# Performance work log

Hardware: AMD Instinct MI355X
Metric: run time of the kernel (lower is better)

## Reference

```python
import jax, jax.numpy as jnp
import numpy as np

N = 50000
E = 600000
IN_DIM = 128
D = 32          # out_dim per head
H = 4           # heads
M = 3           # num metapaths
HID = 128       # semantic attention hidden
NEG_SLOPE = 0.2


def setup_inputs() -> dict:
    key = jax.random.key(0)
    ks = jax.random.split(key, 12)
    x = jax.random.normal(ks[0], (N, IN_DIM), dtype=jnp.float32)
    mp_edge_index = jax.random.randint(ks[1], (M, 2, E), 0, N, dtype=jnp.int64)
    s = 1.0 / np.sqrt(IN_DIM)
    W = jax.random.normal(ks[2], (M, IN_DIM, H * D), dtype=jnp.float32) * s
    att_src = jax.random.normal(ks[3], (M, H, D), dtype=jnp.float32) * (1.0 / np.sqrt(D))
    att_dst = jax.random.normal(ks[4], (M, H, D), dtype=jnp.float32) * (1.0 / np.sqrt(D))
    bias = jnp.zeros((M, H * D), dtype=jnp.float32)
    ln_gamma = jnp.ones((H * D,), dtype=jnp.float32)
    ln_beta = jnp.zeros((H * D,), dtype=jnp.float32)
    sem_W1 = jax.random.normal(ks[5], (H * D, HID), dtype=jnp.float32) * (1.0 / np.sqrt(H * D))
    sem_b1 = jnp.zeros((HID,), dtype=jnp.float32)
    sem_W2 = jax.random.normal(ks[6], (HID, 1), dtype=jnp.float32) * (1.0 / np.sqrt(HID))
    return dict(x=x, mp_edge_index=mp_edge_index, W=W, att_src=att_src,
                att_dst=att_dst, bias=bias, ln_gamma=ln_gamma, ln_beta=ln_beta,
                sem_W1=sem_W1, sem_b1=sem_b1, sem_W2=sem_W2)


def _gat_conv(x, edge_index, W_m, a_src, a_dst, b_m):
    # PyG GATConv (add_self_loops=True, concat=True). x: [N, F_in]
    n = x.shape[0]
    h = (x @ W_m).reshape(n, H, D)                       # [N, H, D]
    loops = jnp.arange(n, dtype=edge_index.dtype)
    src = jnp.concatenate([edge_index[0], loops])        # [E+N]
    dst = jnp.concatenate([edge_index[1], loops])
    alpha_s = jnp.einsum('nhd,hd->nh', h, a_src)         # [N, H]
    alpha_d = jnp.einsum('nhd,hd->nh', h, a_dst)
    e = jax.nn.leaky_relu(alpha_s[src] + alpha_d[dst], NEG_SLOPE)  # [E+N, H]
    # segment softmax over edges grouped by destination node
    e_max = jax.ops.segment_max(e, dst, num_segments=n)
    e = jnp.exp(e - e_max[dst])
    denom = jax.ops.segment_sum(e, dst, num_segments=n)
    alpha = e / (denom[dst] + 1e-16)                     # [E+N, H]
    msg = h[src] * alpha[:, :, None]                     # [E+N, H, D]
    out = jax.ops.segment_sum(msg, dst, num_segments=n)  # [N, H, D]
    return out.reshape(n, H * D) + b_m


def _layer_norm(y, gamma, beta):
    mu = y.mean(-1, keepdims=True)
    var = y.var(-1, keepdims=True)
    return (y - mu) * jax.lax.rsqrt(var + 1e-5) * gamma + beta


def reference(x, mp_edge_index, W, att_src, att_dst, bias, ln_gamma, ln_beta,
              sem_W1, sem_b1, sem_W2):
    embs = []
    for i in range(M):
        emb = _gat_conv(x, mp_edge_index[i], W[i], att_src[i], att_dst[i], bias[i])
        emb = jax.nn.elu(_layer_norm(emb, ln_gamma, ln_beta))
        embs.append(emb)
    z = jnp.stack(embs, axis=1)                          # [N, M, H*D]
    # semantic attention
    w = (jnp.tanh(z @ sem_W1 + sem_b1) @ sem_W2).mean(0)  # [M, 1]
    beta = jax.nn.softmax(w, axis=0)                      # [M, 1]
    out_emb = (beta[None, :, :] * z).sum(1)               # [N, H*D]
    att_mp = beta.squeeze()                               # [M]
    return out_emb, att_mp
```

## Files before the change

kernel.cpp:

```cpp
#include <hip/hip_runtime.h>
#include <hip/hip_bf16.h>

#define N_NODES 50000
#define N_EDGES 600000
#define NMETA   3
#define LTOT (NMETA * N_NODES)
#define SPAN_SHIFT 9
#define NBUCK 98
#define BCAP 8192
#define NCHUNK 147
#define NABLK 782
#define NSLOT (NMETA * NBUCK * BCAP)
#define LOG2E 1.4426950408889634f

typedef unsigned short u16;
typedef short bf16x8 __attribute__((ext_vector_type(8)));
typedef float f32x4 __attribute__((ext_vector_type(4)));

__device__ __forceinline__ float bf2f(u16 v) {
    union { unsigned int u; float f; } x; x.u = ((unsigned int)v) << 16; return x.f;
}
__device__ __forceinline__ float u2f(unsigned int u) {
    union { unsigned int u; float f; } x; x.u = u; return x.f;
}
__device__ __forceinline__ u16 f2bf(float f) {
    return __hip_bfloat16_raw(__float2bfloat16(f)).x;
}

__global__ __launch_bounds__(256) void k_build1(
    const int* __restrict__ ei, int* __restrict__ gcnt,
    unsigned long long* __restrict__ pairs,
    const float* __restrict__ W, const float* __restrict__ W1,
    u16* __restrict__ WT, u16* __restrict__ W1T)
{
    const int bid = blockIdx.x;
    const int t = threadIdx.x;
    if (bid >= NMETA * NCHUNK) {
        int idx = (bid - NMETA * NCHUNK) * 256 + t;
        if (idx < NMETA * 16384) {
            int m = idx >> 14, r = idx & 16383;
            int col = r >> 7, k = r & 127;
            WT[idx] = f2bf(W[(m << 14) + k * 128 + col]);
        } else {
            int r = idx - NMETA * 16384;
            int col = r >> 7, k = r & 127;
            W1T[r] = f2bf(W1[k * 128 + col]);
        }
        return;
    }
    const int m = bid / NCHUNK;
    const int e0 = (bid % NCHUNK) * 4096;
    __shared__ int cnt[NBUCK];
    __shared__ int gbase[NBUCK];
    if (t < NBUCK) cnt[t] = 0;
    __syncthreads();
    const int* srcp = ei + (size_t)m * 2 * N_EDGES;
    const int* dstp = srcp + N_EDGES;
    int sa[16], da[16], sl[16];
    #pragma unroll
    for (int j = 0; j < 16; ++j) {
        int e = e0 + j * 256 + t;
        if (e < N_EDGES) {
            int s = srcp[e], d = dstp[e];
            if ((unsigned)s >= N_NODES) s = 0;
            if ((unsigned)d >= N_NODES) d = 0;
            sa[j] = s; da[j] = d;
            sl[j] = atomicAdd(&cnt[d >> SPAN_SHIFT], 1);
        } else sl[j] = -1;
    }
    __syncthreads();
    if (t < NBUCK) gbase[t] = atomicAdd(&gcnt[m * NBUCK + t], cnt[t]);
    __syncthreads();
    #pragma unroll
    for (int j = 0; j < 16; ++j) {
        if (sl[j] < 0) continue;
        int b = da[j] >> SPAN_SHIFT;
        int pos = gbase[b] + sl[j];
        if (pos < BCAP)
            pairs[(size_t)(m * NBUCK + b) * BCAP + pos] =
                ((unsigned long long)(da[j] & 511) << 32) | (unsigned)(sa[j] * 128);
    }
}

__global__ __launch_bounds__(256) void k_build2(
    const int* __restrict__ gcnt, const unsigned long long* __restrict__ pairs,
    int* __restrict__ row_start, int* __restrict__ row_end, int* __restrict__ eidx,
    int* __restrict__ ptot,
    const float* __restrict__ x, const u16* __restrict__ WT,
    const float* __restrict__ att_src, const float* __restrict__ att_dst,
    u16* __restrict__ h, float* __restrict__ alpha_s, float* __restrict__ alpha_d)
{
    const int bid = blockIdx.x;
    const int t = threadIdx.x;
    if (bid < NMETA * NBUCK) {
        const int m = bid / NBUCK, b = bid % NBUCK;
        __shared__ int cnt[512];
        __shared__ int off[512];
        __shared__ int wsum[4];
        int nb = gcnt[m * NBUCK + b]; if (nb > BCAP) nb = BCAP;
        const int base = (m * NBUCK + b) * BCAP;
        cnt[t] = 0; cnt[t + 256] = 0;
        __syncthreads();
        for (int e = t; e < nb; e += 256) {
            int dl = (int)(pairs[(size_t)base + e] >> 32);
            atomicAdd(&cnt[dl], 1);
        }
        __syncthreads();
        int c0 = cnt[2 * t], c1 = cnt[2 * t + 1];
        int v0p = (c0 + 3) & ~3, v1p = (c1 + 3) & ~3;
        int s = v0p + v1p;
        int lane = t & 63, wv = t >> 6;
        int incl = s;
        #pragma unroll
        for (int o = 1; o < 64; o <<= 1) {
            int u = __shfl_up(incl, o);
            if (lane >= o) incl += u;
        }
        if (lane == 63) wsum[wv] = incl;
        __syncthreads();
        int woff = 0;
        for (int i = 0; i < wv; ++i) woff += wsum[i];
        int ex = woff + incl - s;
        off[2 * t] = ex;
        off[2 * t + 1] = ex + v0p;
        if (t == 255) {
            int tot = ex + v0p + v1p;
            ptot[m * NBUCK + b] = tot < BCAP ? tot : BCAP;
        }
        for (int q = ex + c0; q < ex + v0p && q < BCAP; ++q) eidx[base + q] = 0;
        for (int q = ex + v0p + c1; q < ex + v0p + v1p && q < BCAP; ++q) eidx[base + q] = 0;
        __syncthreads();
        const int node0 = b << SPAN_SHIFT;
        for (int i = t; i < 512; i += 256) {
            int n = node0 + i;
            if (n < N_NODES) {
                int st = base + off[i];
                row_start[m * N_NODES + n] = st;
                row_end[m * N_NODES + n]   = st + cnt[i];
            }
        }
        __syncthreads();
        for (int e = t; e < nb; e += 256) {
            unsigned long long p = pairs[(size_t)base + e];
            int dl = (int)(p >> 32);
            int pos = atomicAdd(&off[dl], 1);
            if (pos >= BCAP) continue;
            eidx[base + pos] = (dl << 23) | (int)(unsigned)p;
        }
        return;
    }
    const int g = bid - NMETA * NBUCK;
    const int bx = g % NABLK, m = g / NABLK;
    const int wv = t >> 6, lane = t & 63;
    const int row0 = (bx * 4 + wv) * 16;
    if (row0 >= N_NODES) return;
    const int lhi = lane >> 4, llo = lane & 15;
    const float* xrow = x + (size_t)(row0 + llo) * 128 + lhi * 8;
    bf16x8 a[4];
    #pragma unroll
    for (int ks = 0; ks < 4; ++ks) {
        float4 f0 = *(const float4*)(xrow + ks * 32);
        float4 f1 = *(const float4*)(xrow + ks * 32 + 4);
        bf16x8 av;
        av[0] = f2bf(f0.x); av[1] = f2bf(f0.y); av[2] = f2bf(f0.z); av[3] = f2bf(f0.w);
        av[4] = f2bf(f1.x); av[5] = f2bf(f1.y); av[6] = f2bf(f1.z); av[7] = f2bf(f1.w);
        a[ks] = av;
    }
    const u16* wbase = WT + (size_t)m * 16384 + (size_t)llo * 128 + lhi * 8;
    u16* hm = h + ((size_t)m * N_NODES + row0) * 128;
    float sp[4][4], dp[4][4];
    #pragma unroll
    for (int i = 0; i < 4; ++i)
        #pragma unroll
        for (int r = 0; r < 4; ++r) { sp[i][r] = 0.f; dp[i][r] = 0.f; }
    #pragma unroll
    for (int cf = 0; cf < 8; ++cf) {
        f32x4 acc = {0.f, 0.f, 0.f, 0.f};
        const u16* wp = wbase + cf * 16 * 128;
        #pragma unroll
        for (int ks = 0; ks < 4; ++ks) {
            bf16x8 bb = *(const bf16x8*)(wp + ks * 32);
            acc = __builtin_amdgcn_mfma_f32_16x16x32_bf16(a[ks], bb, acc, 0, 0, 0);
        }
        const int col = cf * 16 + llo;
        const int hh = cf >> 1;
        const float as = att_src[m * 128 + col];
        const float adv = att_dst[m * 128 + col];
        #pragma unroll
        for (int r = 0; r < 4; ++r) {
            hm[(size_t)(lhi * 4 + r) * 128 + col] = f2bf(acc[r]);
            sp[hh][r] += acc[r] * as;
            dp[hh][r] += acc[r] * adv;
        }
    }
    #pragma unroll
    for (int o = 1; o <= 8; o <<= 1) {
        #pragma unroll
        for (int i = 0; i < 4; ++i)
            #pragma unroll
            for (int r = 0; r < 4; ++r) {
                sp[i][r] += __shfl_xor(sp[i][r], o);
                dp[i][r] += __shfl_xor(dp[i][r], o);
            }
    }
    if (llo == 0) {
        #pragma unroll
        for (int r = 0; r < 4; ++r) {
            int n = row0 + lhi * 4 + r;
            f32x4 vs = {sp[0][r] * LOG2E, sp[1][r] * LOG2E, sp[2][r] * LOG2E, sp[3][r] * LOG2E};
            f32x4 vd = {dp[0][r] * LOG2E, dp[1][r] * LOG2E, dp[2][r] * LOG2E, dp[3][r] * LOG2E};
            *(f32x4*)(alpha_s + ((size_t)m * N_NODES + n) * 4) = vs;
            *(f32x4*)(alpha_d + ((size_t)m * N_NODES + n) * 4) = vd;
        }
    }
}

__global__ __launch_bounds__(256) void k_ew(
    const int* __restrict__ ptot, int* __restrict__ eidx,
    const float* __restrict__ alpha_s, const float* __restrict__ alpha_d,
    u16* __restrict__ ew)
{
    for (int sidx = blockIdx.x * 256 + threadIdx.x; sidx < NSLOT; sidx += gridDim.x * 256) {
        const int bucket = sidx >> 13;
        const int i = sidx & (BCAP - 1);
        if (i >= ptot[bucket]) continue;
        const int m = bucket / NBUCK, b = bucket % NBUCK;
        const int node0 = b << SPAN_SHIFT;
        int v = eidx[sidx];
        int src128 = v & 0x7FFFFF;
        int dl = (unsigned)v >> 23;
        const float* as_m = alpha_s + (size_t)m * N_NODES * 4;
        const float* ad_m = alpha_d + (size_t)m * N_NODES * 4;
        f32x4 as4 = *(const f32x4*)(as_m + (src128 >> 5));
        f32x4 ad4 = *(const f32x4*)(ad_m + (size_t)(node0 + dl) * 4);
        u16* ewp = ew + (size_t)(sidx >> 2) * 16 + (sidx & 3);
        #pragma unroll
        for (int k = 0; k < 4; ++k) {
            float pre = as4[k] + ad4[k];
            pre = fmaxf(pre, 0.2f * pre);
            ewp[k * 4] = f2bf(exp2f(pre));
        }
        eidx[sidx] = src128 * 2;
    }
}

__global__ __launch_bounds__(256) void k_gather(
    const int* __restrict__ row_start, const int* __restrict__ row_end,
    const int* __restrict__ eidx, const u16* __restrict__ ew,
    const float* __restrict__ alpha_s, const float* __restrict__ alpha_d,
    const u16* __restrict__ h,
    const float* __restrict__ bias, const float* __restrict__ gamma,
    const float* __restrict__ lbeta,
    u16* __restrict__ z)
{
    long long w = ((long long)blockIdx.x * blockDim.x + threadIdx.x) >> 6;
    if (w >= (long long)LTOT) return;
    int m = (int)(w / N_NODES), n = (int)(w % N_NODES);
    int lane = threadIdx.x & 63, hh = lane >> 4;
    const char* h_m = (const char*)(h + (size_t)m * N_NODES * 128);
    const char* ewb = (const char*)ew;
    const int lb = lane * 4;
    const float* as_m = alpha_s + (size_t)m * N_NODES * 4;
    const float* ad_m = alpha_d + (size_t)m * N_NODES * 4;
    float pre = as_m[n * 4 + hh] + ad_m[n * 4 + hh];
    pre = fmaxf(pre, 0.2f * pre);
    float ev = exp2f(pre);
    float esum = ev;
    ushort2 hv = *(const ushort2*)(h_m + (size_t)n * 256 + lb);
    float acc0 = ev * bf2f(hv.x), acc1 = ev * bf2f(hv.y);
    int p = row_start[m * N_NODES + n];
    const int end = row_end[m * N_NODES + n];
    for (; p + 3 < end; p += 4) {
        int4 o4 = *(const int4*)(eidx + p);
        uint2 ewv = *(const uint2*)(ewb + (size_t)(p + hh) * 8);
        float e1 = u2f(ewv.x << 16), e2 = u2f(ewv.x & 0xffff0000u);
        float e3 = u2f(ewv.y << 16), e4 = u2f(ewv.y & 0xffff0000u);
        ushort2 h1 = *(const ushort2*)(h_m + o4.x + lb);
        ushort2 h2 = *(const ushort2*)(h_m + o4.y + lb);
        ushort2 h3 = *(const ushort2*)(h_m + o4.z + lb);
        ushort2 h4 = *(const ushort2*)(h_m + o4.w + lb);
        esum += (e1 + e2) + (e3 + e4);
        acc0 += e1 * bf2f(h1.x) + e2 * bf2f(h2.x) + e3 * bf2f(h3.x) + e4 * bf2f(h4.x);
        acc1 += e1 * bf2f(h1.y) + e2 * bf2f(h2.y) + e3 * bf2f(h3.y) + e4 * bf2f(h4.y);
    }
    for (; p < end; ++p) {
        int o1 = eidx[p];
        float e1 = bf2f(*(const u16*)(ewb + (size_t)((p & ~3) + hh) * 8 + (p & 3) * 2));
        ushort2 h1 = *(const ushort2*)(h_m + o1 + lb);
        esum += e1;
        acc0 += e1 * bf2f(h1.x);
        acc1 += e1 * bf2f(h1.y);
    }
    float rinv = 1.f / (esum + 1e-16f);
    float v0 = acc0 * rinv + bias[m * 128 + lane * 2];
    float v1 = acc1 * rinv + bias[m * 128 + lane * 2 + 1];
    float s1 = v0 + v1, s2 = v0 * v0 + v1 * v1;
    #pragma unroll
    for (int o = 32; o >= 1; o >>= 1) { s1 += __shfl_xor(s1, o); s2 += __shfl_xor(s2, o); }
    float mu = s1 * (1.f / 128.f);
    float var = s2 * (1.f / 128.f) - mu * mu;
    float rs = rsqrtf(var + 1e-5f);
    float o0 = (v0 - mu) * rs * gamma[lane * 2]     + lbeta[lane * 2];
    float o1 = (v1 - mu) * rs * gamma[lane * 2 + 1] + lbeta[lane * 2 + 1];
    o0 = o0 > 0.f ? o0 : (__expf(o0) - 1.f);
    o1 = o1 > 0.f ? o1 : (__expf(o1) - 1.f);
    ushort2 outv; outv.x = f2bf(o0); outv.y = f2bf(o1);
    *(ushort2*)(z + ((size_t)n * NMETA + m) * 128 + lane * 2) = outv;
}

__global__ __launch_bounds__(256) void k_sem(
    const u16* __restrict__ z, const u16* __restrict__ W1T,
    const float* __restrict__ b1, const float* __restrict__ W2,
    float* __restrict__ wpart)
{
    __shared__ float part[NMETA];
    const int t = threadIdx.x;
    if (t < NMETA) part[t] = 0.f;
    __syncthreads();
    const int wv = t >> 6, lane = t & 63;
    const int row0 = (blockIdx.x * 4 + wv) * 16;
    if (row0 < LTOT) {
        const int lhi = lane >> 4, llo = lane & 15;
        const u16* zrow = z + (size_t)(row0 + llo) * 128 + lhi * 8;
        bf16x8 a[4];
        #pragma unroll
        for (int ks = 0; ks < 4; ++ks) a[ks] = *(const bf16x8*)(zrow + ks * 32);
        const u16* wb = W1T + (size_t)llo * 128 + lhi * 8;
        float rowacc[4] = {0.f, 0.f, 0.f, 0.f};
        #pragma unroll
        for (int cf = 0; cf < 8; ++cf) {
            f32x4 acc = {0.f, 0.f, 0.f, 0.f};
            const u16* wp = wb + cf * 16 * 128;
            #pragma unroll
            for (int ks = 0; ks < 4; ++ks) {
                bf16x8 bb = *(const bf16x8*)(wp + ks * 32);
                acc = __builtin_amdgcn_mfma_f32_16x16x32_bf16(a[ks], bb, acc, 0, 0, 0);
            }
            int col = cf * 16 + llo;
            float b1v = b1[col], w2v = W2[col];
            #pragma unroll
            for (int r = 0; r < 4; ++r)
                rowacc[r] += tanhf(acc[r] + b1v) * w2v;
        }
        #pragma unroll
        for (int o = 1; o <= 8; o <<= 1) {
            #pragma unroll
            for (int r = 0; r < 4; ++r) rowacc[r] += __shfl_xor(rowacc[r], o);
        }
        if (llo == 0) {
            #pragma unroll
            for (int r = 0; r < 4; ++r)
                atomicAdd(&part[(row0 + lhi * 4 + r) % NMETA], rowacc[r]);
        }
    }
    __syncthreads();
    if (t < NMETA) atomicAdd(&wpart[t], part[t]);
}

__global__ void k_beta(const float* __restrict__ wpart, float* __restrict__ betab,
                       float* __restrict__ attout)
{
    if (threadIdx.x == 0 && blockIdx.x == 0) {
        float w0 = wpart[0] * (1.f / N_NODES);
        float w1 = wpart[1] * (1.f / N_NODES);
        float w2 = wpart[2] * (1.f / N_NODES);
        float mx = fmaxf(w0, fmaxf(w1, w2));
        float e0 = __expf(w0 - mx), e1 = __expf(w1 - mx), e2 = __expf(w2 - mx);
        float s = 1.f / (e0 + e1 + e2);
        float b0 = e0 * s, b1 = e1 * s, b2 = e2 * s;
        betab[0] = b0; betab[1] = b1; betab[2] = b2;
        attout[0] = b0; attout[1] = b1; attout[2] = b2;
    }
}

__global__ __launch_bounds__(256) void k_combine(
    const u16* __restrict__ z, const float* __restrict__ betab,
    float* __restrict__ out)
{
    int idx = blockIdx.x * blockDim.x + threadIdx.x;
    if (idx >= N_NODES * 64) return;
    int n = idx >> 6, c2 = (idx & 63) * 2;
    float b0 = betab[0], b1 = betab[1], b2 = betab[2];
    const u16* zp = z + (size_t)n * NMETA * 128 + c2;
    ushort2 a0 = *(const ushort2*)(zp);
    ushort2 a1 = *(const ushort2*)(zp + 128);
    ushort2 a2 = *(const ushort2*)(zp + 256);
    float2 ov;
    ov.x = b0 * bf2f(a0.x) + b1 * bf2f(a1.x) + b2 * bf2f(a2.x);
    ov.y = b0 * bf2f(a0.y) + b1 * bf2f(a1.y) + b2 * bf2f(a2.y);
    *(float2*)(out + (size_t)n * 128 + c2) = ov;
}

extern "C" void kernel_launch(void* const* d_in, const int* in_sizes, int n_in,
                              void* d_out, int out_size, void* d_ws, size_t ws_size,
                              hipStream_t stream) {
    const float* x       = (const float*)d_in[0];
    const int*   ei      = (const int*)d_in[1];
    const float* W       = (const float*)d_in[2];
    const float* att_src = (const float*)d_in[3];
    const float* att_dst = (const float*)d_in[4];
    const float* bias    = (const float*)d_in[5];
    const float* gamma   = (const float*)d_in[6];
    const float* lbeta   = (const float*)d_in[7];
    const float* W1      = (const float*)d_in[8];
    const float* b1      = (const float*)d_in[9];
    const float* W2      = (const float*)d_in[10];

    char* ws = (char*)d_ws;
    size_t off = 0;
    int* gcnt    = (int*)(ws + off);  off += sizeof(int) * 512;
    int* ptot    = (int*)(ws + off);  off += sizeof(int) * 512;
    float* wpart = (float*)(ws + off);
    float* betab = wpart + 8;         off += 64;
    const size_t zero_bytes = off;
    off = (off + 255) & ~(size_t)255;
    int* row_start = (int*)(ws + off); off += sizeof(int) * 150016;
    int* row_end   = (int*)(ws + off); off += sizeof(int) * 150016;
    u16* h      = (u16*)(ws + off);    off += sizeof(u16) * (size_t)NMETA * N_NODES * 128;
    float* alpha_s = (float*)(ws + off); off += sizeof(float) * (size_t)LTOT * 4;
    float* alpha_d = (float*)(ws + off); off += sizeof(float) * (size_t)LTOT * 4;
    u16* WT     = (u16*)(ws + off);    off += sizeof(u16) * (size_t)NMETA * 128 * 128;
    u16* W1T    = (u16*)(ws + off);    off += sizeof(u16) * (size_t)128 * 128;
    int* eidx   = (int*)(ws + off);    off += sizeof(int) * (size_t)NSLOT;
    u16* ew     = (u16*)(ws + off);    off += sizeof(u16) * (size_t)NSLOT * 4;
    unsigned long long* pairs = (unsigned long long*)(ws + off);
    u16* z = (u16*)(ws + off);
    off += sizeof(u16) * (size_t)N_NODES * NMETA * 128;
    if (ws_size < off) return;

    hipMemsetAsync(d_ws, 0, zero_bytes, stream);

    k_build1<<<dim3(NMETA * NCHUNK + 256), 256, 0, stream>>>(ei, gcnt, pairs, W, W1, WT, W1T);
    k_build2<<<dim3(NMETA * NBUCK + NABLK * NMETA), 256, 0, stream>>>(
        gcnt, pairs, row_start, row_end, eidx, ptot,
        x, WT, att_src, att_dst, h, alpha_s, alpha_d);
    k_ew<<<dim3(2048), 256, 0, stream>>>(ptot, eidx, alpha_s, alpha_d, ew);
    k_gather<<<dim3((LTOT + 3) / 4), 256, 0, stream>>>(row_start, row_end, eidx, ew,
                                                       alpha_s, alpha_d, h,
                                                       bias, gamma, lbeta, z);
    k_sem<<<dim3((LTOT / 16 + 3) / 4), 256, 0, stream>>>(z, W1T, b1, W2, wpart);
    k_beta<<<1, 64, 0, stream>>>(wpart, betab, (float*)d_out + (size_t)N_NODES * 128);
    k_combine<<<dim3((N_NODES * 64 + 255) / 256), 256, 0, stream>>>(z, betab, (float*)d_out);
}
```

Baseline: 279.8 us.

## Pack edge pairs to 32-bit, use bf16 dot2 in gather, fuse beta into semantic kernel

Edge pairs shrink from 64-bit to 32-bit words with the destination-local index pre-shifted, so the bucket sort reads half the bytes and no longer rebuilds the index. The gather loop uses packed bf16 dot2 instructions with byte permutes in place of scalar converts and multiplies. The semantic kernel swaps tanhf for an exp2-based tanh and computes the softmax beta in the last block through an atomic completion counter, removing a separate launch. The combine kernel switches to 16-byte vector loads and stores. The dot2 path accumulates in a different order and the fast tanh is slightly less accurate.

```diff
diff --git a/kernel.cpp b/kernel.cpp
--- a/kernel.cpp
+++ b/kernel.cpp
@@ -11,6 +11,7 @@
 #define NCHUNK 147
 #define NABLK 782
 #define NSLOT (NMETA * NBUCK * BCAP)
+#define NSEMBLK ((LTOT / 16 + 3) / 4)
 #define LOG2E 1.4426950408889634f
 
 typedef unsigned short u16;
@@ -27,9 +28,20 @@
     return __hip_bfloat16_raw(__float2bfloat16(f)).x;
 }
 
+#if __has_builtin(__builtin_amdgcn_fdot2_f32_bf16)
+#define HAS_DOT2 1
+typedef __bf16 bf16x2v __attribute__((ext_vector_type(2)));
+__device__ __forceinline__ float dot2bf(unsigned hp, unsigned ep, float acc) {
+    return __builtin_amdgcn_fdot2_f32_bf16(
+        __builtin_bit_cast(bf16x2v, hp), __builtin_bit_cast(bf16x2v, ep), acc, false);
+}
+#else
+#define HAS_DOT2 0
+#endif
+
 __global__ __launch_bounds__(256) void k_build1(
     const int* __restrict__ ei, int* __restrict__ gcnt,
-    unsigned long long* __restrict__ pairs,
+    unsigned* __restrict__ pairs,
     const float* __restrict__ W, const float* __restrict__ W1,
     u16* __restrict__ WT, u16* __restrict__ W1T)
 {
@@ -78,12 +90,12 @@
         int pos = gbase[b] + sl[j];
         if (pos < BCAP)
             pairs[(size_t)(m * NBUCK + b) * BCAP + pos] =
-                ((unsigned long long)(da[j] & 511) << 32) | (unsigned)(sa[j] * 128);
+                ((unsigned)(da[j] & 511) << 23) | (unsigned)(sa[j] * 128);
     }
 }
 
 __global__ __launch_bounds__(256) void k_build2(
-    const int* __restrict__ gcnt, const unsigned long long* __restrict__ pairs,
+    const int* __restrict__ gcnt, const unsigned* __restrict__ pairs,
     int* __restrict__ row_start, int* __restrict__ row_end, int* __restrict__ eidx,
     int* __restrict__ ptot,
     const float* __restrict__ x, const u16* __restrict__ WT,
@@ -102,7 +114,7 @@
         cnt[t] = 0; cnt[t + 256] = 0;
         __syncthreads();
         for (int e = t; e < nb; e += 256) {
-            int dl = (int)(pairs[(size_t)base + e] >> 32);
+            int dl = (int)(pairs[(size_t)base + e] >> 23);
             atomicAdd(&cnt[dl], 1);
         }
         __syncthreads();
@@ -141,11 +153,11 @@
         }
         __syncthreads();
         for (int e = t; e < nb; e += 256) {
-            unsigned long long p = pairs[(size_t)base + e];
-            int dl = (int)(p >> 32);
+            unsigned pv = pairs[(size_t)base + e];
+            int dl = (int)(pv >> 23);
             int pos = atomicAdd(&off[dl], 1);
             if (pos >= BCAP) continue;
-            eidx[base + pos] = (dl << 23) | (int)(unsigned)p;
+            eidx[base + pos] = (int)pv;
         }
         return;
     }
@@ -266,30 +278,45 @@
     pre = fmaxf(pre, 0.2f * pre);
     float ev = exp2f(pre);
     float esum = ev;
-    ushort2 hv = *(const ushort2*)(h_m + (size_t)n * 256 + lb);
-    float acc0 = ev * bf2f(hv.x), acc1 = ev * bf2f(hv.y);
+    unsigned hv = *(const unsigned*)(h_m + (size_t)n * 256 + lb);
+    float acc0 = ev * u2f(hv << 16), acc1 = ev * u2f(hv & 0xffff0000u);
     int p = row_start[m * N_NODES + n];
     const int end = row_end[m * N_NODES + n];
     for (; p + 3 < end; p += 4) {
         int4 o4 = *(const int4*)(eidx + p);
         uint2 ewv = *(const uint2*)(ewb + (size_t)(p + hh) * 8);
+        unsigned h1 = *(const unsigned*)(h_m + o4.x + lb);
+        unsigned h2 = *(const unsigned*)(h_m + o4.y + lb);
+        unsigned h3 = *(const unsigned*)(h_m + o4.z + lb);
+        unsigned h4 = *(const unsigned*)(h_m + o4.w + lb);
+#if HAS_DOT2
+        unsigned lo12 = __builtin_amdgcn_perm(h2, h1, 0x05040100u);
+        unsigned hi12 = __builtin_amdgcn_perm(h2, h1, 0x07060302u);
+        unsigned lo34 = __builtin_amdgcn_perm(h4, h3, 0x05040100u);
+        unsigned hi34 = __builtin_amdgcn_perm(h4, h3, 0x07060302u);
+        acc0 = dot2bf(lo12, ewv.x, acc0);
+        acc1 = dot2bf(hi12, ewv.x, acc1);
+        acc0 = dot2bf(lo34, ewv.y, acc0);
+        acc1 = dot2bf(hi34, ewv.y, acc1);
+        esum = dot2bf(0x3F803F80u, ewv.x, esum);
+        esum = dot2bf(0x3F803F80u, ewv.y, esum);
+#else
         float e1 = u2f(ewv.x << 16), e2 = u2f(ewv.x & 0xffff0000u);
         float e3 = u2f(ewv.y << 16), e4 = u2f(ewv.y & 0xffff0000u);
-        ushort2 h1 = *(const ushort2*)(h_m + o4.x + lb);
-        ushort2 h2 = *(const ushort2*)(h_m + o4.y + lb);
-        ushort2 h3 = *(const ushort2*)(h_m + o4.z + lb);
-        ushort2 h4 = *(const ushort2*)(h_m + o4.w + lb);
         esum += (e1 + e2) + (e3 + e4);
-        acc0 += e1 * bf2f(h1.x) + e2 * bf2f(h2.x) + e3 * bf2f(h3.x) + e4 * bf2f(h4.x);
-        acc1 += e1 * bf2f(h1.y) + e2 * bf2f(h2.y) + e3 * bf2f(h3.y) + e4 * bf2f(h4.y);
+        acc0 += e1 * u2f(h1 << 16) + e2 * u2f(h2 << 16)
+              + e3 * u2f(h3 << 16) + e4 * u2f(h4 << 16);
+        acc1 += e1 * u2f(h1 & 0xffff0000u) + e2 * u2f(h2 & 0xffff0000u)
+              + e3 * u2f(h3 & 0xffff0000u) + e4 * u2f(h4 & 0xffff0000u);
+#endif
     }
     for (; p < end; ++p) {
         int o1 = eidx[p];
         float e1 = bf2f(*(const u16*)(ewb + (size_t)((p & ~3) + hh) * 8 + (p & 3) * 2));
-        ushort2 h1 = *(const ushort2*)(h_m + o1 + lb);
+        unsigned h1 = *(const unsigned*)(h_m + o1 + lb);
         esum += e1;
-        acc0 += e1 * bf2f(h1.x);
-        acc1 += e1 * bf2f(h1.y);
+        acc0 += e1 * u2f(h1 << 16);
+        acc1 += e1 * u2f(h1 & 0xffff0000u);
     }
     float rinv = 1.f / (esum + 1e-16f);
     float v0 = acc0 * rinv + bias[m * 128 + lane * 2];
@@ -311,7 +338,8 @@
 __global__ __launch_bounds__(256) void k_sem(
     const u16* __restrict__ z, const u16* __restrict__ W1T,
     const float* __restrict__ b1, const float* __restrict__ W2,
-    float* __restrict__ wpart)
+    float* __restrict__ wpart, int* __restrict__ donecnt,
+    float* __restrict__ betab, float* __restrict__ attout)
 {
     __shared__ float part[NMETA];
     const int t = threadIdx.x;
@@ -339,8 +367,11 @@
             int col = cf * 16 + llo;
             float b1v = b1[col], w2v = W2[col];
             #pragma unroll
-            for (int r = 0; r < 4; ++r)
-                rowacc[r] += tanhf(acc[r] + b1v) * w2v;
+            for (int r = 0; r < 4; ++r) {
+                float targ = acc[r] + b1v;
+                float tv = 1.f - 2.f / (exp2f(targ * (2.f * LOG2E)) + 1.f);
+                rowacc[r] += tv * w2v;
+            }
         }
         #pragma unroll
         for (int o = 1; o <= 8; o <<= 1) {
@@ -355,21 +386,22 @@
     }
     __syncthreads();
     if (t < NMETA) atomicAdd(&wpart[t], part[t]);
-}
-
-__global__ void k_beta(const float* __restrict__ wpart, float* __restrict__ betab,
-                       float* __restrict__ attout)
-{
-    if (threadIdx.x == 0 && blockIdx.x == 0) {
-        float w0 = wpart[0] * (1.f / N_NODES);
-        float w1 = wpart[1] * (1.f / N_NODES);
-        float w2 = wpart[2] * (1.f / N_NODES);
-        float mx = fmaxf(w0, fmaxf(w1, w2));
-        float e0 = __expf(w0 - mx), e1 = __expf(w1 - mx), e2 = __expf(w2 - mx);
-        float s = 1.f / (e0 + e1 + e2);
-        float b0 = e0 * s, b1 = e1 * s, b2 = e2 * s;
-        betab[0] = b0; betab[1] = b1; betab[2] = b2;
-        attout[0] = b0; attout[1] = b1; attout[2] = b2;
+    __syncthreads();
+    if (t == 0) {
+        __threadfence();
+        int old = atomicAdd(donecnt, 1);
+        if (old == NSEMBLK - 1) {
+            __threadfence();
+            float w0 = wpart[0] * (1.f / N_NODES);
+            float w1 = wpart[1] * (1.f / N_NODES);
+            float w2 = wpart[2] * (1.f / N_NODES);
+            float mx = fmaxf(w0, fmaxf(w1, w2));
+            float e0 = __expf(w0 - mx), e1 = __expf(w1 - mx), e2 = __expf(w2 - mx);
+            float s = 1.f / (e0 + e1 + e2);
+            float b0 = e0 * s, b1v = e1 * s, b2 = e2 * s;
+            betab[0] = b0; betab[1] = b1v; betab[2] = b2;
+            attout[0] = b0; attout[1] = b1v; attout[2] = b2;
+        }
     }
 }
 
@@ -378,17 +410,26 @@
     float* __restrict__ out)
 {
     int idx = blockIdx.x * blockDim.x + threadIdx.x;
-    if (idx >= N_NODES * 64) return;
-    int n = idx >> 6, c2 = (idx & 63) * 2;
+    if (idx >= N_NODES * 16) return;
+    int n = idx >> 4, c8 = (idx & 15) * 8;
     float b0 = betab[0], b1 = betab[1], b2 = betab[2];
-    const u16* zp = z + (size_t)n * NMETA * 128 + c2;
-    ushort2 a0 = *(const ushort2*)(zp);
-    ushort2 a1 = *(const ushort2*)(zp + 128);
-    ushort2 a2 = *(const ushort2*)(zp + 256);
-    float2 ov;
-    ov.x = b0 * bf2f(a0.x) + b1 * bf2f(a1.x) + b2 * bf2f(a2.x);
-    ov.y = b0 * bf2f(a0.y) + b1 * bf2f(a1.y) + b2 * bf2f(a2.y);
-    *(float2*)(out + (size_t)n * 128 + c2) = ov;
+    const u16* zp = z + (size_t)n * 384 + c8;
+    uint4 a0 = *(const uint4*)(zp);
+    uint4 a1 = *(const uint4*)(zp + 128);
+    uint4 a2 = *(const uint4*)(zp + 256);
+    const unsigned* p0 = (const unsigned*)&a0;
+    const unsigned* p1 = (const unsigned*)&a1;
+    const unsigned* p2 = (const unsigned*)&a2;
+    float o[8];
+    #pragma unroll
+    for (int j = 0; j < 4; ++j) {
+        o[2 * j]     = b0 * u2f(p0[j] << 16) + b1 * u2f(p1[j] << 16) + b2 * u2f(p2[j] << 16);
+        o[2 * j + 1] = b0 * u2f(p0[j] & 0xffff0000u) + b1 * u2f(p1[j] & 0xffff0000u)
+                     + b2 * u2f(p2[j] & 0xffff0000u);
+    }
+    float* op = out + (size_t)n * 128 + c8;
+    *(float4*)(op)     = make_float4(o[0], o[1], o[2], o[3]);
+    *(float4*)(op + 4) = make_float4(o[4], o[5], o[6], o[7]);
 }
 
 extern "C" void kernel_launch(void* const* d_in, const int* in_sizes, int n_in,
@@ -411,7 +452,8 @@
     int* gcnt    = (int*)(ws + off);  off += sizeof(int) * 512;
     int* ptot    = (int*)(ws + off);  off += sizeof(int) * 512;
     float* wpart = (float*)(ws + off);
-    float* betab = wpart + 8;         off += 64;
+    float* betab = wpart + 8;
+    int* donecnt = (int*)(betab + 8); off += 128;
     const size_t zero_bytes = off;
     off = (off + 255) & ~(size_t)255;
     int* row_start = (int*)(ws + off); off += sizeof(int) * 150016;
@@ -423,7 +465,7 @@
     u16* W1T    = (u16*)(ws + off);    off += sizeof(u16) * (size_t)128 * 128;
     int* eidx   = (int*)(ws + off);    off += sizeof(int) * (size_t)NSLOT;
     u16* ew     = (u16*)(ws + off);    off += sizeof(u16) * (size_t)NSLOT * 4;
-    unsigned long long* pairs = (unsigned long long*)(ws + off);
+    unsigned* pairs = (unsigned*)(ws + off);
     u16* z = (u16*)(ws + off);
     off += sizeof(u16) * (size_t)N_NODES * NMETA * 128;
     if (ws_size < off) return;
@@ -438,7 +480,7 @@
     k_gather<<<dim3((LTOT + 3) / 4), 256, 0, stream>>>(row_start, row_end, eidx, ew,
                                                        alpha_s, alpha_d, h,
                                                        bias, gamma, lbeta, z);
-    k_sem<<<dim3((LTOT / 16 + 3) / 4), 256, 0, stream>>>(z, W1T, b1, W2, wpart);
-    k_beta<<<1, 64, 0, stream>>>(wpart, betab, (float*)d_out + (size_t)N_NODES * 128);
-    k_combine<<<dim3((N_NODES * 64 + 255) / 256), 256, 0, stream>>>(z, betab, (float*)d_out);
-}
+    k_sem<<<dim3(NSEMBLK), 256, 0, stream>>>(z, W1T, b1, W2, wpart, donecnt,
+                                             betab, (float*)d_out + (size_t)N_NODES * 128);
+    k_combine<<<dim3((N_NODES * 16 + 255) / 256), 256, 0, stream>>>(z, betab, (float*)d_out);
+}
```

New measurement: 309.8 us. 10.7% more time.
